# Kernel tuning notes

Measured on AMD Instinct MI355X. Metric: run time of the kernel, lower is better.

## Reference

```python
import jax, jax.numpy as jnp
import numpy as np

BSZ, SL, K, D = 4, 2048, 24, 512  # batch, seq len, num_eigh, d_out (=d_in)


def _top_hankel_eigh(sl: int, k: int):
    # Hankel matrix Z[i,j] = 2 / ((i+j)^3 - (i+j)), 1-indexed i,j in [sl]
    idx = np.arange(1, sl + 1, dtype=np.float64)
    s = idx[:, None] + idx[None, :]
    Z = 2.0 / (s ** 3 - s)
    evals, evecs = np.linalg.eigh(Z)  # ascending
    eig_vals = jnp.asarray(evals[-k:], dtype=jnp.float32)       # [k]
    eig_vecs = jnp.asarray(evecs[:, -k:], dtype=jnp.float32)    # [sl, k]
    return eig_vals, eig_vecs


def setup_inputs() -> dict:
    key = jax.random.key(0)
    k1, k2 = jax.random.split(key)
    eig_vals, eig_vecs = _top_hankel_eigh(SL, K)
    inputs = jax.random.normal(k1, (BSZ, SL, D), dtype=jnp.float32)
    m_phi = jax.random.normal(k2, (D * K, D), dtype=jnp.float32) * 0.02
    return {"inputs": inputs, "eig_vals": eig_vals, "eig_vecs": eig_vecs, "m_phi": m_phi}


def _compute_x_tilde(inputs, eig_vals, eig_vecs):
    # Causal convolution of each input channel with each Hankel eigenvector,
    # done via FFT: out[b,t,i,d] = sum_{s<=t} v[s,i] * u[b,t-s,d]
    bsz, sl, d = inputs.shape
    k = eig_vals.shape[0]
    n = 2 * sl  # zero-pad to avoid circular wraparound
    V_f = jnp.fft.rfft(eig_vecs, n=n, axis=0)          # [n//2+1, k]
    U_f = jnp.fft.rfft(inputs, n=n, axis=1)            # [bsz, n//2+1, d]
    prod = V_f[None, :, :, None] * U_f[:, :, None, :]  # [bsz, n//2+1, k, d]
    conv = jnp.fft.irfft(prod, n=n, axis=1)[:, :sl]    # [bsz, sl, k, d]
    x_tilde = conv * (eig_vals ** 0.25)[None, None, :, None]
    return x_tilde.reshape(bsz, sl, k * d)             # [bsz, sl, k*d]


def reference(inputs, eig_vals, eig_vecs, m_phi):
    # dropout layers are identity in eval / p=0
    x_tilde = _compute_x_tilde(inputs, eig_vals, eig_vecs)
    return x_tilde @ m_phi                             # [bsz, sl, d_out]
```

## Files before the change

kernel.cpp:

```cpp
#include <hip/hip_runtime.h>

typedef _Float16 f16;
typedef _Float16 f16x8 __attribute__((ext_vector_type(8)));
typedef float    f32x4 __attribute__((ext_vector_type(4)));

#define BSZ 4
#define SL  2048
#define NK  24
#define DD  512
#define NPP 134
#define KI  8

typedef const void GV __attribute__((address_space(1)));
typedef void       LV __attribute__((address_space(3)));

__device__ __forceinline__ void gload_lds16(const void* gp, void* lp) {
  __builtin_amdgcn_global_load_lds((GV*)gp, (LV*)lp, 16, 0, 0);
}

__global__ void k_afrag(const float* __restrict__ eig_vals,
                        const float* __restrict__ eig_vecs,
                        f16* __restrict__ afrag) {
  int i = blockIdx.x, pp = blockIdx.y;
  int l = threadIdx.x;
  float sc = sqrtf(sqrtf(eig_vals[i]));
  int base = 2047 - 16 * (pp - 6) - (l & 15) + 8 * (l >> 4);
  f16 tmp[8];
#pragma unroll
  for (int j = 0; j < 8; ++j) {
    int x = base + j;
    float v = (x >= 0 && x < SL) ? eig_vecs[(size_t)(SL - 1 - x) * NK + i] * sc : 0.f;
    tmp[j] = (f16)v;
  }
  *(f16x8*)(afrag + (((size_t)i * NPP + pp) * 64 + l) * 8) = *(const f16x8*)tmp;
}

__global__ void k_tu(const float* __restrict__ u, f16* __restrict__ ut) {
  __shared__ float tile[32][33];
  int b = blockIdx.z;
  int s0 = blockIdx.x * 32, d0 = blockIdx.y * 32;
  int tx = threadIdx.x, ty = threadIdx.y;
#pragma unroll
  for (int r = 0; r < 4; ++r) {
    int s = s0 + ty * 4 + r;
    tile[ty * 4 + r][tx] = u[((size_t)b * SL + s) * DD + d0 + tx];
  }
  __syncthreads();
#pragma unroll
  for (int r = 0; r < 4; ++r) {
    int d = d0 + ty * 4 + r;
    ut[((size_t)b * DD + d) * SL + s0 + tx] = (f16)tile[tx][ty * 4 + r];
  }
}

__global__ void k_tm(const float* __restrict__ mp, f16* __restrict__ mht) {
  __shared__ float tile[32][33];
  int k0 = blockIdx.x * 32, e0 = blockIdx.y * 32;
  int tx = threadIdx.x, ty = threadIdx.y;
#pragma unroll
  for (int r = 0; r < 4; ++r)
    tile[ty * 4 + r][tx] = mp[(size_t)(k0 + ty * 4 + r) * DD + e0 + tx];
  __syncthreads();
#pragma unroll
  for (int r = 0; r < 4; ++r)
    mht[(size_t)(e0 + ty * 4 + r) * (NK * DD) + k0 + tx] = (f16)tile[tx][ty * 4 + r];
}

__global__ __launch_bounds__(256, 2) void k_conv(
    const f16* __restrict__ ut, const f16* __restrict__ afrag,
    f16* __restrict__ xt, int ibase) {
  __shared__ f16 bt[3][256 * 32];
  const int tid = threadIdx.x;
  const int lin = blockIdx.x + (blockIdx.y << 5) + (blockIdx.z << 8);
  const int tb = (lin >> 6) & 15;
  const int dh = lin & 1;
  const int iL = (lin >> 1) & 7;
  const int b  = (lin >> 4) & 3;
  const int iG = ibase + iL;
  const int t0 = tb * 128;

  const int w = tid >> 6, l = tid & 63;
  const int l15 = l & 15, lq = l >> 4;
  const int stage_col = ((l & 3) ^ ((l >> 3) & 3)) * 8;
  const int stage_row = l >> 2;
  const int rd_x = (lq ^ ((l15 >> 1) & 3)) * 16;

  const f16* utb = ut + (size_t)b * DD * SL;
  const f16* afi = afrag + ((size_t)iG * NPP * 64 + l) * 8;

  auto stage = [&](int buf, int s0) {
#pragma unroll
    for (int j = 0; j < 4; ++j) {
      int row = w * 64 + j * 16 + stage_row;
      gload_lds16(utb + (size_t)(dh * 256 + row) * SL + s0 + stage_col,
                  &bt[buf][(w * 64 + j * 16) * 32]);
    }
  };

  f32x4 acc[8][4];
#pragma unroll
  for (int m = 0; m < 8; ++m)
#pragma unroll
    for (int n = 0; n < 4; ++n) acc[m][n] = (f32x4){0.f, 0.f, 0.f, 0.f};

  const int nIter = 4 * (tb + 1);
  int pp0 = 8 * tb + 6;

  stage(0, 0);
  f16x8 A[8];
#pragma unroll
  for (int m = 0; m < 8; ++m)
    A[m] = *(const f16x8*)(afi + (size_t)(pp0 + m) * 512);
  stage(1, 32);
  asm volatile("s_waitcnt vmcnt(4)" ::: "memory");
  __builtin_amdgcn_s_barrier();
  __builtin_amdgcn_sched_barrier(0);

  int ra = 0;
  for (int it = 0; it < nIter; it += 2) {
    f16x8 B0[4];
#pragma unroll
    for (int n = 0; n < 4; ++n) {
      int row = w * 64 + n * 16 + l15;
      B0[n] = *(const f16x8*)((const char*)&bt[ra][0] + row * 64 + rd_x);
    }
    int ppn = pp0 - 2; if (ppn < 0) ppn = 0;
    const f16* fpt = afi + (size_t)ppn * 512;
    f16x8 f0 = *(const f16x8*)fpt;
    f16x8 f1 = *(const f16x8*)(fpt + 512);
    int sa = ra + 2; if (sa >= 3) sa -= 3;
    if (it + 2 < nIter) stage(sa, (it + 2) * 32);

    asm volatile("s_waitcnt vmcnt(6)" ::: "memory");
    __builtin_amdgcn_s_barrier();
    __builtin_amdgcn_sched_barrier(0);

    __builtin_amdgcn_s_setprio(1);
#pragma unroll
    for (int m = 0; m < 8; ++m)
#pragma unroll
      for (int n = 0; n < 4; ++n)
        acc[m][n] = __builtin_amdgcn_mfma_f32_16x16x32_f16(A[m], B0[n], acc[m][n], 0, 0, 0);
    __builtin_amdgcn_s_setprio(0);

    int rb = ra + 1; if (rb >= 3) rb -= 3;
    f16x8 B1[4];
#pragma unroll
    for (int n = 0; n < 4; ++n) {
      int row = w * 64 + n * 16 + l15;
      B1[n] = *(const f16x8*)((const char*)&bt[rb][0] + row * 64 + rd_x);
    }
    int pp2 = pp0 - 4; if (pp2 < 0) pp2 = 0;
    const f16* gpt = afi + (size_t)pp2 * 512;
    f16x8 g0 = *(const f16x8*)gpt;
    f16x8 g1 = *(const f16x8*)(gpt + 512);
    if (it + 3 < nIter) stage(ra, (it + 3) * 32);

    asm volatile("s_waitcnt vmcnt(6)" ::: "memory");
    __builtin_amdgcn_s_barrier();
    __builtin_amdgcn_sched_barrier(0);

    __builtin_amdgcn_s_setprio(1);
#pragma unroll
    for (int n = 0; n < 4; ++n) {
      acc[0][n] = __builtin_amdgcn_mfma_f32_16x16x32_f16(f0, B1[n], acc[0][n], 0, 0, 0);
      acc[1][n] = __builtin_amdgcn_mfma_f32_16x16x32_f16(f1, B1[n], acc[1][n], 0, 0, 0);
#pragma unroll
      for (int m = 2; m < 8; ++m)
        acc[m][n] = __builtin_amdgcn_mfma_f32_16x16x32_f16(A[m - 2], B1[n], acc[m][n], 0, 0, 0);
    }
    __builtin_amdgcn_s_setprio(0);

    A[7] = A[3]; A[6] = A[2]; A[5] = A[1]; A[4] = A[0];
    A[3] = f1;   A[2] = f0;   A[1] = g1;   A[0] = g0;
    pp0 -= 4;
    ra = rb + 1; if (ra >= 3) ra -= 3;
  }

  const size_t rowlen = (size_t)KI * DD;
  const int dbase = dh * 256 + w * 64;
#pragma unroll
  for (int m = 0; m < 8; ++m) {
    int t = t0 + m * 16 + lq * 4;
#pragma unroll
    for (int n = 0; n < 4; ++n) {
      int d = dbase + n * 16 + l15;
      f16* dst = xt + ((size_t)(b * SL + t) * KI + iL) * DD + d;
#pragma unroll
      for (int r = 0; r < 4; ++r)
        dst[(size_t)r * rowlen] = (f16)acc[m][n][r];
    }
  }
}

__global__ __launch_bounds__(256, 2) void k_gemm(
    const f16* __restrict__ xt, const f16* __restrict__ mht,
    float* __restrict__ out, int kc0, int beta) {
  __shared__ f16 at[3][64 * 64];
  __shared__ f16 btl[3][128 * 64];
  const int AK = KI * DD;
  const int tid = threadIdx.x;
  const int n0 = blockIdx.x * 128;
  const int m0 = blockIdx.y * 64;
  const int w = tid >> 6, l = tid & 63;
  const int l15 = l & 15, lq = l >> 4;
  const int wm = w >> 1, wn = w & 1;
  const int stage_col = ((l & 7) ^ (l >> 3)) * 8;
  const int stage_row = l >> 3;

  auto stage = [&](int buf, int k0) {
#pragma unroll
    for (int j = 0; j < 2; ++j) {
      int row = (w * 2 + j) * 8 + stage_row;
      gload_lds16(xt + (size_t)(m0 + row) * AK + k0 + stage_col,
                  &at[buf][(w * 2 + j) * 8 * 64]);
    }
#pragma unroll
    for (int j = 0; j < 4; ++j) {
      int row = (w * 4 + j) * 8 + stage_row;
      gload_lds16(mht + (size_t)(n0 + row) * (NK * DD) + kc0 + k0 + stage_col,
                  &btl[buf][(w * 4 + j) * 8 * 64]);
    }
  };

  f32x4 acc[2][4];
#pragma unroll
  for (int m = 0; m < 2; ++m)
#pragma unroll
    for (int n = 0; n < 4; ++n) acc[m][n] = (f32x4){0.f, 0.f, 0.f, 0.f};

  const int nIter = AK / 64;
  stage(0, 0);
  stage(1, 64);
  asm volatile("s_waitcnt vmcnt(6)" ::: "memory");
  __builtin_amdgcn_s_barrier();
  __builtin_amdgcn_sched_barrier(0);

  for (int it = 0; it < nIter; ++it) {
    const int bufR = it % 3;
    f16x8 Af[2][2], Bf[2][4];
#pragma unroll
    for (int ks = 0; ks < 2; ++ks) {
#pragma unroll
      for (int m = 0; m < 2; ++m) {
        int lin2 = (wm * 32 + m * 16 + l15) * 128 + ks * 64 + lq * 16;
        lin2 ^= (l15 & 7) << 4;
        Af[ks][m] = *(const f16x8*)((const char*)&at[bufR][0] + lin2);
      }
#pragma unroll
      for (int n = 0; n < 4; ++n) {
        int lin2 = (wn * 64 + n * 16 + l15) * 128 + ks * 64 + lq * 16;
        lin2 ^= (l15 & 7) << 4;
        Bf[ks][n] = *(const f16x8*)((const char*)&btl[bufR][0] + lin2);
      }
    }

    if (it + 2 < nIter) stage((it + 2) % 3, (it + 2) * 64);

    asm volatile("s_waitcnt vmcnt(6)" ::: "memory");
    __builtin_amdgcn_s_barrier();
    __builtin_amdgcn_sched_barrier(0);

    __builtin_amdgcn_s_setprio(1);
#pragma unroll
    for (int ks = 0; ks < 2; ++ks)
#pragma unroll
      for (int m = 0; m < 2; ++m)
#pragma unroll
        for (int n = 0; n < 4; ++n)
          acc[m][n] = __builtin_amdgcn_mfma_f32_16x16x32_f16(
              Af[ks][m], Bf[ks][n], acc[m][n], 0, 0, 0);
    __builtin_amdgcn_s_setprio(0);
  }

#pragma unroll
  for (int m = 0; m < 2; ++m) {
    int row = m0 + wm * 32 + m * 16 + lq * 4;
#pragma unroll
    for (int n = 0; n < 4; ++n) {
      int e = n0 + wn * 64 + n * 16 + l15;
      float* dst = out + (size_t)row * DD + e;
#pragma unroll
      for (int r = 0; r < 4; ++r) {
        float v = acc[m][n][r];
        if (beta) v += dst[(size_t)r * DD];
        dst[(size_t)r * DD] = v;
      }
    }
  }
}

extern "C" void kernel_launch(void* const* d_in, const int* in_sizes, int n_in,
                              void* d_out, int out_size, void* d_ws, size_t ws_size,
                              hipStream_t stream) {
  const float* u    = (const float*)d_in[0];
  const float* ev   = (const float*)d_in[1];
  const float* evec = (const float*)d_in[2];
  const float* mp   = (const float*)d_in[3];
  float* out = (float*)d_out;
  char* ws = (char*)d_ws;

  const size_t UT_OFF  = 0;
  const size_t MHT_OFF = 8388608;
  const size_t AF_OFF  = 20971520;
  const size_t XT_OFF  = 24264704;

  f16* ut    = (f16*)(ws + UT_OFF);
  f16* mht   = (f16*)(ws + MHT_OFF);
  f16* afrag = (f16*)(ws + AF_OFF);
  f16* xt    = (f16*)(ws + XT_OFF);

  k_afrag<<<dim3(24, NPP), 64, 0, stream>>>(ev, evec, afrag);
  k_tu<<<dim3(SL / 32, DD / 32, BSZ), dim3(32, 8), 0, stream>>>(u, ut);
  k_tm<<<dim3((NK * DD) / 32, DD / 32), dim3(32, 8), 0, stream>>>(mp, mht);

  for (int c = 0; c < NK / KI; ++c) {
    k_conv<<<dim3(32, KI, BSZ), 256, 0, stream>>>(ut, afrag, xt, c * KI);
    k_gemm<<<dim3(DD / 128, (BSZ * SL) / 64), 256, 0, stream>>>(
        xt, mht, out, c * KI * DD, c > 0);
  }
}
```

Measured before the change: 397.4 us.

## Enlarge GEMM tile to 128x128 with K-step 32 and new LDS swizzle

Changes the GEMM block tile from 64x128 to 128x128 so each wave computes a 64x64 sub-tile (4x4 MFMA accumulators), which raises arithmetic intensity per loaded byte. The K step drops from 64 to 32 to keep LDS use per buffer small, and the staging layout and XOR swizzle are redone for 32-wide rows. Launch bounds drop to one block per SIMD group, and the grid halves to 256 blocks, which reduces occupancy and parallelism on a large-CU GPU. The loop now drains fully with vmcnt(0) on the final iterations.

```diff
diff --git a/kernel.cpp b/kernel.cpp
--- a/kernel.cpp
+++ b/kernel.cpp
@@ -193,89 +193,81 @@
   }
 }
 
-__global__ __launch_bounds__(256, 2) void k_gemm(
+__global__ __launch_bounds__(256, 1) void k_gemm(
     const f16* __restrict__ xt, const f16* __restrict__ mht,
     float* __restrict__ out, int kc0, int beta) {
-  __shared__ f16 at[3][64 * 64];
-  __shared__ f16 btl[3][128 * 64];
+  __shared__ f16 at[3][128 * 32];
+  __shared__ f16 btl[3][128 * 32];
   const int AK = KI * DD;
   const int tid = threadIdx.x;
   const int n0 = blockIdx.x * 128;
-  const int m0 = blockIdx.y * 64;
+  const int m0 = blockIdx.y * 128;
   const int w = tid >> 6, l = tid & 63;
   const int l15 = l & 15, lq = l >> 4;
   const int wm = w >> 1, wn = w & 1;
-  const int stage_col = ((l & 7) ^ (l >> 3)) * 8;
-  const int stage_row = l >> 3;
+  const int stage_col = ((l & 3) ^ ((l >> 3) & 3)) * 8;
+  const int stage_row = l >> 2;
+  const int rd_x = (lq ^ ((l15 >> 1) & 3)) * 16;
 
   auto stage = [&](int buf, int k0) {
 #pragma unroll
     for (int j = 0; j < 2; ++j) {
-      int row = (w * 2 + j) * 8 + stage_row;
+      int row = w * 32 + j * 16 + stage_row;
       gload_lds16(xt + (size_t)(m0 + row) * AK + k0 + stage_col,
-                  &at[buf][(w * 2 + j) * 8 * 64]);
-    }
-#pragma unroll
-    for (int j = 0; j < 4; ++j) {
-      int row = (w * 4 + j) * 8 + stage_row;
+                  &at[buf][(w * 32 + j * 16) * 32]);
       gload_lds16(mht + (size_t)(n0 + row) * (NK * DD) + kc0 + k0 + stage_col,
-                  &btl[buf][(w * 4 + j) * 8 * 64]);
+                  &btl[buf][(w * 32 + j * 16) * 32]);
     }
   };
 
-  f32x4 acc[2][4];
-#pragma unroll
-  for (int m = 0; m < 2; ++m)
+  f32x4 acc[4][4];
+#pragma unroll
+  for (int m = 0; m < 4; ++m)
 #pragma unroll
     for (int n = 0; n < 4; ++n) acc[m][n] = (f32x4){0.f, 0.f, 0.f, 0.f};
 
-  const int nIter = AK / 64;
+  const int nIter = AK / 32;
   stage(0, 0);
-  stage(1, 64);
-  asm volatile("s_waitcnt vmcnt(6)" ::: "memory");
+  stage(1, 32);
+  asm volatile("s_waitcnt vmcnt(4)" ::: "memory");
   __builtin_amdgcn_s_barrier();
   __builtin_amdgcn_sched_barrier(0);
 
   for (int it = 0; it < nIter; ++it) {
     const int bufR = it % 3;
-    f16x8 Af[2][2], Bf[2][4];
-#pragma unroll
-    for (int ks = 0; ks < 2; ++ks) {
-#pragma unroll
-      for (int m = 0; m < 2; ++m) {
-        int lin2 = (wm * 32 + m * 16 + l15) * 128 + ks * 64 + lq * 16;
-        lin2 ^= (l15 & 7) << 4;
-        Af[ks][m] = *(const f16x8*)((const char*)&at[bufR][0] + lin2);
-      }
-#pragma unroll
-      for (int n = 0; n < 4; ++n) {
-        int lin2 = (wn * 64 + n * 16 + l15) * 128 + ks * 64 + lq * 16;
-        lin2 ^= (l15 & 7) << 4;
-        Bf[ks][n] = *(const f16x8*)((const char*)&btl[bufR][0] + lin2);
-      }
-    }
-
-    if (it + 2 < nIter) stage((it + 2) % 3, (it + 2) * 64);
-
-    asm volatile("s_waitcnt vmcnt(6)" ::: "memory");
+    f16x8 Af[4], Bf[4];
+#pragma unroll
+    for (int m = 0; m < 4; ++m) {
+      int row = wm * 64 + m * 16 + l15;
+      Af[m] = *(const f16x8*)((const char*)&at[bufR][0] + row * 64 + rd_x);
+    }
+#pragma unroll
+    for (int n = 0; n < 4; ++n) {
+      int row = wn * 64 + n * 16 + l15;
+      Bf[n] = *(const f16x8*)((const char*)&btl[bufR][0] + row * 64 + rd_x);
+    }
+
+    if (it + 2 < nIter) {
+      stage((it + 2) % 3, (it + 2) * 32);
+      asm volatile("s_waitcnt vmcnt(4)" ::: "memory");
+    } else {
+      asm volatile("s_waitcnt vmcnt(0)" ::: "memory");
+    }
     __builtin_amdgcn_s_barrier();
     __builtin_amdgcn_sched_barrier(0);
 
     __builtin_amdgcn_s_setprio(1);
 #pragma unroll
-    for (int ks = 0; ks < 2; ++ks)
-#pragma unroll
-      for (int m = 0; m < 2; ++m)
-#pragma unroll
-        for (int n = 0; n < 4; ++n)
-          acc[m][n] = __builtin_amdgcn_mfma_f32_16x16x32_f16(
-              Af[ks][m], Bf[ks][n], acc[m][n], 0, 0, 0);
+    for (int m = 0; m < 4; ++m)
+#pragma unroll
+      for (int n = 0; n < 4; ++n)
+        acc[m][n] = __builtin_amdgcn_mfma_f32_16x16x32_f16(Af[m], Bf[n], acc[m][n], 0, 0, 0);
     __builtin_amdgcn_s_setprio(0);
   }
 
 #pragma unroll
-  for (int m = 0; m < 2; ++m) {
-    int row = m0 + wm * 32 + m * 16 + lq * 4;
+  for (int m = 0; m < 4; ++m) {
+    int row = m0 + wm * 64 + m * 16 + lq * 4;
 #pragma unroll
     for (int n = 0; n < 4; ++n) {
       int e = n0 + wn * 64 + n * 16 + l15;
@@ -316,7 +308,7 @@
 
   for (int c = 0; c < NK / KI; ++c) {
     k_conv<<<dim3(32, KI, BSZ), 256, 0, stream>>>(ut, afrag, xt, c * KI);
-    k_gemm<<<dim3(DD / 128, (BSZ * SL) / 64), 256, 0, stream>>>(
+    k_gemm<<<dim3(DD / 128, (BSZ * SL) / 128), 256, 0, stream>>>(
         xt, mht, out, c * KI * DD, c > 0);
   }
 }
```

Measured after the change: 478.8 us. +20.5%, slower.
